# Optimization experiments

Measured on AMD Instinct MI355X. Metric: run time of the kernel, lower is better.

Reference implementation:

```python
import jax, jax.numpy as jnp
import numpy as np

N_NODES = 100000
N_EDGES = 1600000
IN_DIM = 64
HID = 64
N_LAYERS = 2
BN_EPS = 1e-5


def setup_inputs() -> dict:
    key = jax.random.key(0)
    ks = jax.random.split(key, 10)
    s = 0.02
    return {
        "x": jax.random.normal(ks[0], (N_NODES, IN_DIM), dtype=jnp.float32),
        "edge_index": jax.random.randint(ks[1], (2, N_EDGES), 0, N_NODES),
        "edge_attr": jax.random.uniform(ks[2], (N_EDGES,), dtype=jnp.float32),
        "lin_W": jax.random.normal(ks[3], (IN_DIM, HID), dtype=jnp.float32) * s,
        "lin_b": jnp.zeros((HID,), dtype=jnp.float32),
        "eenc_w": jax.random.normal(ks[4], (HID,), dtype=jnp.float32) * s,
        "eenc_b": jnp.zeros((HID,), dtype=jnp.float32),
        "conv_W": jax.random.normal(ks[5], (N_LAYERS, HID, HID), dtype=jnp.float32) * s,
        "conv_b": jnp.zeros((N_LAYERS, HID), dtype=jnp.float32),
        "bn_gamma": jnp.ones((N_LAYERS, HID), dtype=jnp.float32),
        "bn_beta": jnp.zeros((N_LAYERS, HID), dtype=jnp.float32),
    }


def _forward(x, edge_index, edge_attr, lin_W, lin_b, eenc_w, eenc_b,
             conv_W, conv_b, bn_gamma, bn_beta):
    n = x.shape[0]
    src, dst = edge_index[0], edge_index[1]
    # input projection (in_dim > 1 -> lin_layer branch)
    h = x @ lin_W + lin_b                                  # [N, HID]
    e = edge_attr[:, None] * eenc_w[None, :] + eenc_b      # [E, HID]
    h0 = h
    h = h.at[src].set(jax.nn.relu(h0[src] + e))
    h = h.at[dst].set(jax.nn.relu(h0[dst] + e))
    # GCN normalization with self-loops (weight 1), shared across layers
    loops = jnp.arange(n)
    s2 = jnp.concatenate([src, loops])
    d2 = jnp.concatenate([dst, loops])
    w2 = jnp.concatenate([edge_attr, jnp.ones((n,), dtype=h.dtype)])
    deg = jax.ops.segment_sum(w2, d2, num_segments=n)
    dinv = jnp.where(deg > 0, 1.0 / jnp.sqrt(jnp.where(deg > 0, deg, 1.0)), 0.0)
    norm = dinv[s2] * w2 * dinv[d2]                        # [E+N]
    h_list = []
    for l in range(N_LAYERS):
        xw = h @ conv_W[l]                                 # [N, HID]
        agg = jax.ops.segment_sum(norm[:, None] * xw[s2], d2, num_segments=n)
        agg = agg + conv_b[l]
        mean = jnp.mean(agg, axis=0)
        var = jnp.mean((agg - mean) ** 2, axis=0)          # biased, as BN uses
        hn = (agg - mean) / jnp.sqrt(var + BN_EPS) * bn_gamma[l] + bn_beta[l]
        # dropout is identity (eval mode); relu on all but last layer
        h = hn if l == N_LAYERS - 1 else jax.nn.relu(hn)
        h_list.append(h)
    return jnp.concatenate(h_list, axis=1)                 # [N, N_LAYERS*HID]


def reference(x, edge_index, edge_attr, lin_W, lin_b, eenc_w, eenc_b,
              conv_W, conv_b, bn_gamma, bn_beta):
    return _forward(x, edge_index, edge_attr, lin_W, lin_b, eenc_w, eenc_b,
                    conv_W, conv_b, bn_gamma, bn_beta)
```

## Files before the change

### kernel.cpp

```cpp
#include <hip/hip_runtime.h>
#include <hip/hip_fp16.h>

#define N_NODES 100000
#define N_EDGES 1600000
#define BN_EPS 1e-5f
#define NBLK_E 6250
#define NBLK_G 3125
#define NBLK_N 391
#define NBINS 391
#define BCAP 4608
#define PT 4096
#define NPART 391
#define OVF_CAP 32768
#define A18 262144.0f
#define A18_INV 3.814697265625e-6f
typedef unsigned long long ull;
typedef unsigned int uint;


__global__ void init_kernel(int* gcnt, int* win, uint* zbitmap, int* flags, float* bnacc) {
    int v = blockIdx.x * blockDim.x + threadIdx.x;
    if (v < N_NODES) win[v] = -1;
    if (v < NBINS) gcnt[v] = 0;
    if (v < 3125) zbitmap[v] = 0;
    if (v < 2) flags[v] = 0;
    if (v < 256) bnacc[v] = 0.0f;
}

__launch_bounds__(256)
__global__ void partition_gemm(const int* __restrict__ src, const int* __restrict__ dst,
                               const float* __restrict__ attr,
                               ull* __restrict__ bucket, int* __restrict__ gcnt,
                               int* __restrict__ flags, int* __restrict__ ovf_b,
                               ull* __restrict__ ovf_e,
                               const float* __restrict__ x, const float* __restrict__ lin_W,
                               const float* __restrict__ lin_b, float* __restrict__ h0) {
    __shared__ ull ent[PT];
    __shared__ unsigned short ebin[PT];
    __shared__ int hist[NBINS];
    __shared__ int cur[NBINS];
    __shared__ int gdel[NBINS];
    __shared__ int sc[512];
    int t = threadIdx.x;
    if (blockIdx.x < NPART) {
        int e0 = blockIdx.x * PT;
        int n = N_EDGES - e0; if (n > PT) n = PT;
        for (int b = t; b < NBINS; b += 256) hist[b] = 0;
        __syncthreads();
        for (int k = t; k < n; k += 256) atomicAdd(&hist[dst[e0 + k] >> 8], 1);
        __syncthreads();
        sc[t] = (t < NBINS) ? hist[t] : 0;
        sc[t + 256] = (t + 256 < NBINS) ? hist[t + 256] : 0;
        __syncthreads();
        for (int off = 1; off < 512; off <<= 1) {
            int a0 = sc[t] + ((t >= off) ? sc[t - off] : 0);
            int a1 = sc[t + 256] + sc[t + 256 - off];
            __syncthreads();
            sc[t] = a0; sc[t + 256] = a1;
            __syncthreads();
        }
        for (int b = t; b < NBINS; b += 256) {
            int lb = sc[b] - hist[b];
            cur[b] = lb;
            int gb = atomicAdd(&gcnt[b], hist[b]);
            gdel[b] = gb - lb;
        }
        __syncthreads();
        for (int k = t; k < n; k += 256) {
            int i = e0 + k;
            int d = dst[i];
            uint aq = (uint)(attr[i] * A18); if (aq > 0x3FFFFu) aq = 0x3FFFFu;
            int bin = d >> 8;
            ull e = ((ull)(d & 255) << 56) | ((ull)i << 35) | ((ull)src[i] << 18) | aq;
            int p = atomicAdd(&cur[bin], 1);
            ent[p] = e;
            ebin[p] = (unsigned short)bin;
        }
        __syncthreads();
        for (int k = t; k < n; k += 256) {
            int b = ebin[k];
            int off = k + gdel[b];
            if (off < BCAP) bucket[(size_t)b * BCAP + off] = ent[k];
            else {
                int q = atomicAdd(&flags[1], 1);
                if (q < OVF_CAP) { ovf_b[q] = b; ovf_e[q] = ent[k]; }
            }
        }
        return;
    }
    float* xs = (float*)ent;
    int lane = t & 63, w = t >> 6;
    int base = (blockIdx.x - NPART) * 32;
    const float4* Xv = (const float4*)(x + (size_t)base * 64);
    float4* xsv = (float4*)xs;
    xsv[t] = Xv[t];
    xsv[t + 256] = Xv[t + 256];
    float wc[64];
    #pragma unroll
    for (int k = 0; k < 64; ++k) wc[k] = lin_W[k * 64 + lane];
    __syncthreads();
    float bval = lin_b[lane];
    for (int rr = 0; rr < 8; ++rr) {
        int rl = w * 8 + rr;
        const float4* xr = (const float4*)(xs + rl * 64);
        float acc = bval;
        #pragma unroll
        for (int k4 = 0; k4 < 16; ++k4) {
            float4 xv = xr[k4];
            acc = fmaf(xv.x, wc[4 * k4 + 0], acc);
            acc = fmaf(xv.y, wc[4 * k4 + 1], acc);
            acc = fmaf(xv.z, wc[4 * k4 + 2], acc);
            acc = fmaf(xv.w, wc[4 * k4 + 3], acc);
        }
        h0[(size_t)(base + rl) * 64 + lane] = acc;
    }
}

__launch_bounds__(256)
__global__ void finalize_reorder(const ull* __restrict__ bucket, const int* __restrict__ gcnt,
                                 const int* __restrict__ ovf_b, const ull* __restrict__ ovf_e,
                                 int* __restrict__ flags, uint* __restrict__ zbitmap,
                                 float* __restrict__ dinv, float* __restrict__ wa,
                                 ull* __restrict__ csr2, int* __restrict__ startv,
                                 int* __restrict__ lenv) {
    __shared__ ull ent[BCAP];
    __shared__ int cnt[256];
    __shared__ int sc[256];
    __shared__ int cur[256];
    __shared__ int cbase[257];
    int t = threadIdx.x, b = blockIdx.x;
    int len = gcnt[b], blen = len < BCAP ? len : BCAP;
    const ull* bb = bucket + (size_t)b * BCAP;
    cnt[t] = 0;
    __syncthreads();
    ull r[18];
    #pragma unroll
    for (int k = 0; k < 18; ++k) {
        int j = k * 256 + t;
        r[k] = 0;
        if (j < blen) {
            ull e = bb[j];
            r[k] = e;
            atomicAdd(&cnt[(int)(e >> 56)], 1);
        }
    }
    __syncthreads();
    sc[t] = cnt[t];
    __syncthreads();
    for (int off = 1; off < 256; off <<= 1) {
        int a = sc[t] + ((t >= off) ? sc[t - off] : 0);
        __syncthreads();
        sc[t] = a;
        __syncthreads();
    }
    cbase[t + 1] = sc[t];
    if (t == 0) cbase[0] = 0;
    cur[t] = sc[t] - cnt[t];
    __syncthreads();
    #pragma unroll
    for (int k = 0; k < 18; ++k) {
        int j = k * 256 + t;
        if (j < blen) {
            ull e = r[k];
            int p = atomicAdd(&cur[(int)(e >> 56)], 1);
            ent[p] = e;
        }
    }
    __syncthreads();
    size_t base = (size_t)b * BCAP;
    for (int k = t; k < blen; k += 256) {
        ull e = ent[k];
        csr2[base + k] = (((ull)(e & 0x3FFFFull)) << 32) | ((e >> 18) & 0x1FFFFull);
    }
    int j0 = cbase[t], j1 = cbase[t + 1];
    float sum = 0.0f; uint winx = 0, wat = 0;
    for (int j = j0; j < j1; ++j) {
        ull e = ent[j];
        uint aq = (uint)(e & 0x3FFFFull);
        sum += (float)aq * A18_INV;
        uint ei = (uint)((e >> 35) & 0x1FFFFFull) + 1u;
        if (ei > winx) { winx = ei; wat = aq; }
    }
    if (len > BCAP) {
        int oc = flags[1]; if (oc > OVF_CAP) oc = OVF_CAP;
        for (int q = 0; q < oc; ++q) {
            if (ovf_b[q] != b) continue;
            ull e = ovf_e[q];
            if ((int)(e >> 56) != t) continue;
            uint aq = (uint)(e & 0x3FFFFull);
            sum += (float)aq * A18_INV;
            uint ei = (uint)((e >> 35) & 0x1FFFFFull) + 1u;
            if (ei > winx) { winx = ei; wat = aq; }
        }
    }
    int v = b * 256 + t;
    if (v < N_NODES) {
        dinv[v] = rsqrtf(1.0f + sum);
        startv[v] = (int)(base + j0);
        lenv[v] = j1 - j0;
        if (winx > 0) {
            wa[v] = (float)wat * A18_INV;
        } else {
            wa[v] = -1.0f;
            atomicOr(&zbitmap[v >> 5], 1u << (v & 31));
            flags[0] = 1;
        }
    }
}

__global__ void fixup_scan(const int* __restrict__ src, const int* __restrict__ flags,
                           const uint* __restrict__ zbitmap, int* __restrict__ win) {
    if (flags[0] == 0) return;
    int i = blockIdx.x * 256 + threadIdx.x;
    int s = src[i];
    if ((zbitmap[s >> 5] >> (s & 31)) & 1u) atomicMax(&win[s], i);
}

__global__ void fixup_apply(const int* __restrict__ flags, const uint* __restrict__ zbitmap,
                            const int* __restrict__ win, const float* __restrict__ attr,
                            float* __restrict__ wa) {
    if (flags[0] == 0) return;
    int v = blockIdx.x * 256 + threadIdx.x;
    if (v >= N_NODES) return;
    if (((zbitmap[v >> 5] >> (v & 31)) & 1u) && win[v] >= 0) wa[v] = attr[win[v]];
}

__launch_bounds__(256)
__global__ void gemm_l0_nrm(const float* __restrict__ h0, const float* __restrict__ W,
                            const float* __restrict__ wa, const float* __restrict__ ew,
                            const float* __restrict__ eb, __half* __restrict__ xw16,
                            ull* __restrict__ csr2, const int* __restrict__ gcnt,
                            const float* __restrict__ dinv) {
    __shared__ float xs[2048];
    int t = threadIdx.x;
    if (blockIdx.x < NBINS) {
        int b = blockIdx.x;
        int len = gcnt[b], blen = len < BCAP ? len : BCAP;
        ull* c = csr2 + (size_t)b * BCAP;
        for (int k = t; k < blen; k += 256) {
            ull pk = c[k];
            uint s = (uint)pk;
            float np = (float)(uint)(pk >> 32) * A18_INV * dinv[s];
            c[k] = ((ull)__float_as_uint(np) << 32) | s;
        }
        return;
    }
    int lane = t & 63, w = t >> 6;
    int base = (blockIdx.x - NBINS) * 32;
    const float4* Hv = (const float4*)(h0 + (size_t)base * 64);
    #pragma unroll
    for (int q = 0; q < 2; ++q) {
        int idx = t + q * 256;
        int rl = idx >> 4, f0 = (idx & 15) * 4;
        float4 v = Hv[idx];
        float wav = wa[base + rl];
        if (wav >= 0.0f) {
            v.x = fmaxf(fmaf(wav, ew[f0 + 0], v.x + eb[f0 + 0]), 0.0f);
            v.y = fmaxf(fmaf(wav, ew[f0 + 1], v.y + eb[f0 + 1]), 0.0f);
            v.z = fmaxf(fmaf(wav, ew[f0 + 2], v.z + eb[f0 + 2]), 0.0f);
            v.w = fmaxf(fmaf(wav, ew[f0 + 3], v.w + eb[f0 + 3]), 0.0f);
        }
        ((float4*)xs)[idx] = v;
    }
    float wc[64];
    #pragma unroll
    for (int k = 0; k < 64; ++k) wc[k] = W[k * 64 + lane];
    __syncthreads();
    for (int rr = 0; rr < 8; ++rr) {
        int rl = w * 8 + rr;
        const float4* xr = (const float4*)(xs + rl * 64);
        float acc = 0.0f;
        #pragma unroll
        for (int k4 = 0; k4 < 16; ++k4) {
            float4 xv = xr[k4];
            acc = fmaf(xv.x, wc[4 * k4 + 0], acc);
            acc = fmaf(xv.y, wc[4 * k4 + 1], acc);
            acc = fmaf(xv.z, wc[4 * k4 + 2], acc);
            acc = fmaf(xv.w, wc[4 * k4 + 3], acc);
        }
        xw16[(size_t)(base + rl) * 64 + lane] = __float2half(acc);
    }
}

__launch_bounds__(256)
__global__ void gemm_l1(const float* __restrict__ agg, const float* __restrict__ bnacc,
                        const float* __restrict__ gamma, const float* __restrict__ beta,
                        const float* __restrict__ W, float* __restrict__ out,
                        __half* __restrict__ xw16) {
    __shared__ float xs[2048];
    int t = threadIdx.x, lane = t & 63, w = t >> 6;
    int base = blockIdx.x * 32;
    const float4* Av = (const float4*)(agg + (size_t)base * 64);
    const float invN = 1.0f / (float)N_NODES;
    #pragma unroll
    for (int q = 0; q < 2; ++q) {
        int idx = t + q * 256;
        int rl = idx >> 4, f0 = (idx & 15) * 4;
        float4 v = Av[idx];
        float vv[4] = {v.x, v.y, v.z, v.w};
        #pragma unroll
        for (int c = 0; c < 4; ++c) {
            int f = f0 + c;
            float mean = bnacc[f] * invN;
            float var = bnacc[64 + f] * invN - mean * mean;
            float scl = gamma[f] * rsqrtf(var + BN_EPS);
            float bs = beta[f] - mean * scl;
            vv[c] = fmaxf(fmaf(vv[c], scl, bs), 0.0f);
        }
        float4 r = {vv[0], vv[1], vv[2], vv[3]};
        ((float4*)xs)[idx] = r;
        *(float4*)(out + (size_t)(base + rl) * 128 + f0) = r;
    }
    float wc[64];
    #pragma unroll
    for (int k = 0; k < 64; ++k) wc[k] = W[k * 64 + lane];
    __syncthreads();
    for (int rr = 0; rr < 8; ++rr) {
        int rl = w * 8 + rr;
        const float4* xr = (const float4*)(xs + rl * 64);
        float acc = 0.0f;
        #pragma unroll
        for (int k4 = 0; k4 < 16; ++k4) {
            float4 xv = xr[k4];
            acc = fmaf(xv.x, wc[4 * k4 + 0], acc);
            acc = fmaf(xv.y, wc[4 * k4 + 1], acc);
            acc = fmaf(xv.z, wc[4 * k4 + 2], acc);
            acc = fmaf(xv.w, wc[4 * k4 + 3], acc);
        }
        xw16[(size_t)(base + rl) * 64 + lane] = __float2half(acc);
    }
}

__launch_bounds__(256)
__global__ void gather4(const __half* __restrict__ xw16, const ull* __restrict__ csr2,
                        const int* __restrict__ startv, const int* __restrict__ lenv,
                        const float* __restrict__ dinv, const int* __restrict__ gcnt,
                        const int* __restrict__ flags, const int* __restrict__ ovf_b,
                        const ull* __restrict__ ovf_e,
                        const float* __restrict__ convb, float* __restrict__ agg,
                        float* __restrict__ bnacc) {
    __shared__ float reds[4][64];
    __shared__ float redq[4][64];
    int t = threadIdx.x, lane = t & 63, w = t >> 6;
    int ng = lane >> 4, fl = lane & 15, f0 = fl * 4, ngb = ng << 4;
    float cb0 = convb[f0], cb1 = convb[f0 + 1], cb2 = convb[f0 + 2], cb3 = convb[f0 + 3];
    float s0 = 0.f, s1 = 0.f, s2 = 0.f, s3 = 0.f;
    float q0 = 0.f, q1 = 0.f, q2 = 0.f, q3 = 0.f;
    int ovfn = flags[1];
    for (int v = blockIdx.x * 16 + w * 4 + ng; v < N_NODES; v += 32768) {
        float dv = dinv[v];
        int sb = startv[v], ln = lenv[v];
        float2 raw = *(const float2*)(xw16 + (size_t)v * 64 + f0);
        float2 xv01 = __half22float2(*(__half2*)&raw.x);
        float2 xv23 = __half22float2(*(__half2*)&raw.y);
        float w2 = dv * dv;
        float a0 = w2 * xv01.x, a1 = w2 * xv01.y, a2 = w2 * xv23.x, a3 = w2 * xv23.y;
        float b0 = 0.f, b1 = 0.f, b2 = 0.f, b3 = 0.f;
        for (int c0 = 0; c0 < ln; c0 += 16) {
            int m = ln - c0; if (m > 16) m = 16;
            ull pk = (fl < m) ? csr2[sb + c0 + fl] : 0ull;
            int j = 0;
            for (; j + 4 <= m; j += 4) {
                ull pA = __shfl(pk, ngb + j, 64);
                ull pB = __shfl(pk, ngb + j + 1, 64);
                ull pC = __shfl(pk, ngb + j + 2, 64);
                ull pD = __shfl(pk, ngb + j + 3, 64);
                float2 rA = *(const float2*)(xw16 + (size_t)(uint)pA * 64 + f0);
                float2 rB = *(const float2*)(xw16 + (size_t)(uint)pB * 64 + f0);
                float2 rC = *(const float2*)(xw16 + (size_t)(uint)pC * 64 + f0);
                float2 rD = *(const float2*)(xw16 + (size_t)(uint)pD * 64 + f0);
                float nA = __uint_as_float((uint)(pA >> 32)) * dv;
                float nB = __uint_as_float((uint)(pB >> 32)) * dv;
                float nC = __uint_as_float((uint)(pC >> 32)) * dv;
                float nD = __uint_as_float((uint)(pD >> 32)) * dv;
                float2 xA01 = __half22float2(*(__half2*)&rA.x);
                float2 xA23 = __half22float2(*(__half2*)&rA.y);
                float2 xB01 = __half22float2(*(__half2*)&rB.x);
                float2 xB23 = __half22float2(*(__half2*)&rB.y);
                float2 xC01 = __half22float2(*(__half2*)&rC.x);
                float2 xC23 = __half22float2(*(__half2*)&rC.y);
                float2 xD01 = __half22float2(*(__half2*)&rD.x);
                float2 xD23 = __half22float2(*(__half2*)&rD.y);
                a0 = fmaf(nA, xA01.x, a0); a1 = fmaf(nA, xA01.y, a1);
                a2 = fmaf(nA, xA23.x, a2); a3 = fmaf(nA, xA23.y, a3);
                b0 = fmaf(nB, xB01.x, b0); b1 = fmaf(nB, xB01.y, b1);
                b2 = fmaf(nB, xB23.x, b2); b3 = fmaf(nB, xB23.y, b3);
                a0 = fmaf(nC, xC01.x, a0); a1 = fmaf(nC, xC01.y, a1);
                a2 = fmaf(nC, xC23.x, a2); a3 = fmaf(nC, xC23.y, a3);
                b0 = fmaf(nD, xD01.x, b0); b1 = fmaf(nD, xD01.y, b1);
                b2 = fmaf(nD, xD23.x, b2); b3 = fmaf(nD, xD23.y, b3);
            }
            for (; j < m; ++j) {
                ull pA = __shfl(pk, ngb + j, 64);
                float2 rA = *(const float2*)(xw16 + (size_t)(uint)pA * 64 + f0);
                float nA = __uint_as_float((uint)(pA >> 32)) * dv;
                float2 xA01 = __half22float2(*(__half2*)&rA.x);
                float2 xA23 = __half22float2(*(__half2*)&rA.y);
                a0 = fmaf(nA, xA01.x, a0); a1 = fmaf(nA, xA01.y, a1);
                a2 = fmaf(nA, xA23.x, a2); a3 = fmaf(nA, xA23.y, a3);
            }
        }
        float t0 = a0 + b0, t1 = a1 + b1, t2 = a2 + b2, t3 = a3 + b3;
        if (ovfn > 0 && gcnt[v >> 8] > BCAP) {
            int oc = ovfn; if (oc > OVF_CAP) oc = OVF_CAP;
            int ld = v & 255, b = v >> 8;
            for (int q = 0; q < oc; ++q) {
                if (ovf_b[q] != b) continue;
                ull e = ovf_e[q];
                if ((int)(e >> 56) != ld) continue;
                uint s = (uint)((e >> 18) & 0x1FFFFull);
                float nr = (float)(uint)(e & 0x3FFFFull) * A18_INV * dinv[s] * dv;
                float2 rr = *(const float2*)(xw16 + (size_t)s * 64 + f0);
                float2 x01 = __half22float2(*(__half2*)&rr.x);
                float2 x23 = __half22float2(*(__half2*)&rr.y);
                t0 = fmaf(nr, x01.x, t0); t1 = fmaf(nr, x01.y, t1);
                t2 = fmaf(nr, x23.x, t2); t3 = fmaf(nr, x23.y, t3);
            }
        }
        t0 += cb0; t1 += cb1; t2 += cb2; t3 += cb3;
        *(float4*)(agg + (size_t)v * 64 + f0) = make_float4(t0, t1, t2, t3);
        s0 += t0; q0 += t0 * t0;
        s1 += t1; q1 += t1 * t1;
        s2 += t2; q2 += t2 * t2;
        s3 += t3; q3 += t3 * t3;
    }
    s0 += __shfl_xor(s0, 16, 64); s0 += __shfl_xor(s0, 32, 64);
    s1 += __shfl_xor(s1, 16, 64); s1 += __shfl_xor(s1, 32, 64);
    s2 += __shfl_xor(s2, 16, 64); s2 += __shfl_xor(s2, 32, 64);
    s3 += __shfl_xor(s3, 16, 64); s3 += __shfl_xor(s3, 32, 64);
    q0 += __shfl_xor(q0, 16, 64); q0 += __shfl_xor(q0, 32, 64);
    q1 += __shfl_xor(q1, 16, 64); q1 += __shfl_xor(q1, 32, 64);
    q2 += __shfl_xor(q2, 16, 64); q2 += __shfl_xor(q2, 32, 64);
    q3 += __shfl_xor(q3, 16, 64); q3 += __shfl_xor(q3, 32, 64);
    if (ng == 0) {
        reds[w][f0] = s0; reds[w][f0 + 1] = s1; reds[w][f0 + 2] = s2; reds[w][f0 + 3] = s3;
        redq[w][f0] = q0; redq[w][f0 + 1] = q1; redq[w][f0 + 2] = q2; redq[w][f0 + 3] = q3;
    }
    __syncthreads();
    if (t < 64) {
        float ss = reds[0][t] + reds[1][t] + reds[2][t] + reds[3][t];
        float qq = redq[0][t] + redq[1][t] + redq[2][t] + redq[3][t];
        atomicAdd(&bnacc[t], ss);
        atomicAdd(&bnacc[64 + t], qq);
    }
}

__launch_bounds__(256)
__global__ void bn_final(const float* __restrict__ agg, const float* __restrict__ bnacc,
                         const float* __restrict__ gamma, const float* __restrict__ beta,
                         float* __restrict__ out) {
    int idx = blockIdx.x * 256 + threadIdx.x;
    int f0 = (idx & 15) * 4, v = idx >> 4;
    const float invN = 1.0f / (float)N_NODES;
    float4 a = *(const float4*)(agg + (size_t)v * 64 + f0);
    float r[4] = {a.x, a.y, a.z, a.w};
    #pragma unroll
    for (int c = 0; c < 4; ++c) {
        int f = f0 + c;
        float mean = bnacc[f] * invN;
        float var = bnacc[64 + f] * invN - mean * mean;
        float scl = gamma[f] * rsqrtf(var + BN_EPS);
        float bs = beta[f] - mean * scl;
        r[c] = fmaf(r[c], scl, bs);
    }
    *(float4*)(out + (size_t)v * 128 + 64 + f0) = make_float4(r[0], r[1], r[2], r[3]);
}

extern "C" void kernel_launch(void* const* d_in, const int* in_sizes, int n_in,
                              void* d_out, int out_size, void* d_ws, size_t ws_size,
                              hipStream_t stream) {
    const float* x      = (const float*)d_in[0];
    const int*   eidx   = (const int*)d_in[1];
    const float* attr   = (const float*)d_in[2];
    const float* lin_W  = (const float*)d_in[3];
    const float* lin_b  = (const float*)d_in[4];
    const float* eenc_w = (const float*)d_in[5];
    const float* eenc_b = (const float*)d_in[6];
    const float* conv_W = (const float*)d_in[7];
    const float* conv_b = (const float*)d_in[8];
    const float* gamma  = (const float*)d_in[9];
    const float* beta   = (const float*)d_in[10];
    float* out = (float*)d_out;

    const int* src = eidx;
    const int* dst = eidx + N_EDGES;

    char* p = (char*)d_ws;
    ull* bucket = (ull*)p;   p += (size_t)NBINS * BCAP * 8;
    ull* csr2   = (ull*)p;   p += (size_t)NBINS * BCAP * 8;
    ull* ovf_e  = (ull*)p;   p += (size_t)OVF_CAP * 8;
    float* h0   = (float*)p; p += (size_t)N_NODES * 64 * 4;
    __half* xw16 = (__half*)p; p += (size_t)N_NODES * 64 * 2;
    float* dinv = (float*)p; p += (size_t)N_NODES * 4;
    float* wa   = (float*)p; p += (size_t)N_NODES * 4;
    int* win    = (int*)p;   p += (size_t)N_NODES * 4;
    int* startv = (int*)p;   p += (size_t)N_NODES * 4;
    int* lenv   = (int*)p;   p += (size_t)N_NODES * 4;
    int* ovf_b  = (int*)p;   p += (size_t)OVF_CAP * 4;
    int* gcnt   = (int*)p;   p += (NBINS + 1) * 4 + 20;
    uint* zbitmap = (uint*)p; p += 3125 * 4 + 12;
    int* flags  = (int*)p;   p += 64;
    float* bnacc = (float*)p; p += 256 * 4;
    float* agg = h0;

    init_kernel<<<NBLK_N, 256, 0, stream>>>(gcnt, win, zbitmap, flags, bnacc);
    partition_gemm<<<NPART + NBLK_G, 256, 0, stream>>>(src, dst, attr, bucket, gcnt,
                                                       flags, ovf_b, ovf_e,
                                                       x, lin_W, lin_b, h0);
    finalize_reorder<<<NBINS, 256, 0, stream>>>(bucket, gcnt, ovf_b, ovf_e,
                                                flags, zbitmap, dinv, wa,
                                                csr2, startv, lenv);
    fixup_scan<<<NBLK_E, 256, 0, stream>>>(src, flags, zbitmap, win);
    fixup_apply<<<NBLK_N, 256, 0, stream>>>(flags, zbitmap, win, attr, wa);

    gemm_l0_nrm<<<NBINS + NBLK_G, 256, 0, stream>>>(h0, conv_W, wa, eenc_w, eenc_b,
                                                    xw16, csr2, gcnt, dinv);
    gather4<<<2048, 256, 0, stream>>>(xw16, csr2, startv, lenv, dinv, gcnt,
                                      flags, ovf_b, ovf_e, conv_b, agg, bnacc);
    gemm_l1<<<NBLK_G, 256, 0, stream>>>(agg, bnacc, gamma, beta,
                                        conv_W + 64 * 64, out, xw16);
    gather4<<<2048, 256, 0, stream>>>(xw16, csr2, startv, lenv, dinv, gcnt,
                                      flags, ovf_b, ovf_e, conv_b + 64, agg, bnacc + 128);
    bn_final<<<6250, 256, 0, stream>>>(agg, bnacc + 128, gamma + 64, beta + 64, out);
}
```

Baseline: 415.3 us.

## Store h0 and agg intermediates in fp16 and split gather into node-per-thread launches

Intermediate node features h0 and the aggregation buffer are now stored as fp16 instead of fp32, which halves the bytes written and re-read by the GEMM, gather and BN kernels. The gather kernel drops its grid-stride loop: each thread group now handles one node, and the kernel is launched twice over the two halves of the node range. The partition pass keeps the dst indices in registers so they are not loaded twice. The trade-offs are fp16 rounding of pre-BN values, which can cost accuracy, and two extra kernel launches.

Result: slower. 660.9 us (+59.1%).

```diff
diff --git a/kernel.cpp b/kernel.cpp
--- a/kernel.cpp
+++ b/kernel.cpp
@@ -34,7 +34,7 @@
                                int* __restrict__ flags, int* __restrict__ ovf_b,
                                ull* __restrict__ ovf_e,
                                const float* __restrict__ x, const float* __restrict__ lin_W,
-                               const float* __restrict__ lin_b, float* __restrict__ h0) {
+                               const float* __restrict__ lin_b, __half* __restrict__ h0h) {
     __shared__ ull ent[PT];
     __shared__ unsigned short ebin[PT];
     __shared__ int hist[NBINS];
@@ -47,7 +47,14 @@
         int n = N_EDGES - e0; if (n > PT) n = PT;
         for (int b = t; b < NBINS; b += 256) hist[b] = 0;
         __syncthreads();
-        for (int k = t; k < n; k += 256) atomicAdd(&hist[dst[e0 + k] >> 8], 1);
+        int dreg[16];
+        #pragma unroll
+        for (int i2 = 0; i2 < 16; ++i2) {
+            int k = t + i2 * 256;
+            int d = (k < n) ? dst[e0 + k] : -1;
+            dreg[i2] = d;
+            if (d >= 0) atomicAdd(&hist[d >> 8], 1);
+        }
         __syncthreads();
         sc[t] = (t < NBINS) ? hist[t] : 0;
         sc[t + 256] = (t + 256 < NBINS) ? hist[t + 256] : 0;
@@ -66,9 +73,12 @@
             gdel[b] = gb - lb;
         }
         __syncthreads();
-        for (int k = t; k < n; k += 256) {
+        #pragma unroll
+        for (int i2 = 0; i2 < 16; ++i2) {
+            int k = t + i2 * 256;
+            int d = dreg[i2];
+            if (d < 0) continue;
             int i = e0 + k;
-            int d = dst[i];
             uint aq = (uint)(attr[i] * A18); if (aq > 0x3FFFFu) aq = 0x3FFFFu;
             int bin = d >> 8;
             ull e = ((ull)(d & 255) << 56) | ((ull)i << 35) | ((ull)src[i] << 18) | aq;
@@ -112,7 +122,7 @@
             acc = fmaf(xv.z, wc[4 * k4 + 2], acc);
             acc = fmaf(xv.w, wc[4 * k4 + 3], acc);
         }
-        h0[(size_t)(base + rl) * 64 + lane] = acc;
+        h0h[(size_t)(base + rl) * 64 + lane] = __float2half(acc);
     }
 }
 
@@ -226,7 +236,7 @@
 }
 
 __launch_bounds__(256)
-__global__ void gemm_l0_nrm(const float* __restrict__ h0, const float* __restrict__ W,
+__global__ void gemm_l0_nrm(const __half* __restrict__ h0h, const float* __restrict__ W,
                             const float* __restrict__ wa, const float* __restrict__ ew,
                             const float* __restrict__ eb, __half* __restrict__ xw16,
                             ull* __restrict__ csr2, const int* __restrict__ gcnt,
@@ -247,12 +257,15 @@
     }
     int lane = t & 63, w = t >> 6;
     int base = (blockIdx.x - NBINS) * 32;
-    const float4* Hv = (const float4*)(h0 + (size_t)base * 64);
+    const uint2* Hv = (const uint2*)(h0h + (size_t)base * 64);
     #pragma unroll
     for (int q = 0; q < 2; ++q) {
         int idx = t + q * 256;
         int rl = idx >> 4, f0 = (idx & 15) * 4;
-        float4 v = Hv[idx];
+        uint2 hv = Hv[idx];
+        float2 p01 = __half22float2(*(__half2*)&hv.x);
+        float2 p23 = __half22float2(*(__half2*)&hv.y);
+        float4 v = {p01.x, p01.y, p23.x, p23.y};
         float wav = wa[base + rl];
         if (wav >= 0.0f) {
             v.x = fmaxf(fmaf(wav, ew[f0 + 0], v.x + eb[f0 + 0]), 0.0f);
@@ -283,21 +296,23 @@
 }
 
 __launch_bounds__(256)
-__global__ void gemm_l1(const float* __restrict__ agg, const float* __restrict__ bnacc,
+__global__ void gemm_l1(const __half* __restrict__ aggh, const float* __restrict__ bnacc,
                         const float* __restrict__ gamma, const float* __restrict__ beta,
                         const float* __restrict__ W, float* __restrict__ out,
                         __half* __restrict__ xw16) {
     __shared__ float xs[2048];
     int t = threadIdx.x, lane = t & 63, w = t >> 6;
     int base = blockIdx.x * 32;
-    const float4* Av = (const float4*)(agg + (size_t)base * 64);
+    const uint2* Av = (const uint2*)(aggh + (size_t)base * 64);
     const float invN = 1.0f / (float)N_NODES;
     #pragma unroll
     for (int q = 0; q < 2; ++q) {
         int idx = t + q * 256;
         int rl = idx >> 4, f0 = (idx & 15) * 4;
-        float4 v = Av[idx];
-        float vv[4] = {v.x, v.y, v.z, v.w};
+        uint2 hv = Av[idx];
+        float2 p01 = __half22float2(*(__half2*)&hv.x);
+        float2 p23 = __half22float2(*(__half2*)&hv.y);
+        float vv[4] = {p01.x, p01.y, p23.x, p23.y};
         #pragma unroll
         for (int c = 0; c < 4; ++c) {
             int f = f0 + c;
@@ -332,98 +347,97 @@
 }
 
 __launch_bounds__(256)
-__global__ void gather4(const __half* __restrict__ xw16, const ull* __restrict__ csr2,
+__global__ void gather4(int vbase,
+                        const __half* __restrict__ xw16, const ull* __restrict__ csr2,
                         const int* __restrict__ startv, const int* __restrict__ lenv,
                         const float* __restrict__ dinv, const int* __restrict__ gcnt,
                         const int* __restrict__ flags, const int* __restrict__ ovf_b,
                         const ull* __restrict__ ovf_e,
-                        const float* __restrict__ convb, float* __restrict__ agg,
+                        const float* __restrict__ convb, __half* __restrict__ aggh,
                         float* __restrict__ bnacc) {
     __shared__ float reds[4][64];
     __shared__ float redq[4][64];
     int t = threadIdx.x, lane = t & 63, w = t >> 6;
     int ng = lane >> 4, fl = lane & 15, f0 = fl * 4, ngb = ng << 4;
-    float cb0 = convb[f0], cb1 = convb[f0 + 1], cb2 = convb[f0 + 2], cb3 = convb[f0 + 3];
-    float s0 = 0.f, s1 = 0.f, s2 = 0.f, s3 = 0.f;
-    float q0 = 0.f, q1 = 0.f, q2 = 0.f, q3 = 0.f;
+    int v = vbase + blockIdx.x * 16 + w * 4 + ng;
+    float dv = dinv[v];
+    int sb = startv[v], ln = lenv[v];
+    float2 raw = *(const float2*)(xw16 + (size_t)v * 64 + f0);
+    float2 xv01 = __half22float2(*(__half2*)&raw.x);
+    float2 xv23 = __half22float2(*(__half2*)&raw.y);
+    float w2 = dv * dv;
+    float a0 = w2 * xv01.x, a1 = w2 * xv01.y, a2 = w2 * xv23.x, a3 = w2 * xv23.y;
+    float b0 = 0.f, b1 = 0.f, b2 = 0.f, b3 = 0.f;
+    for (int c0 = 0; c0 < ln; c0 += 16) {
+        int m = ln - c0; if (m > 16) m = 16;
+        ull pk = (fl < m) ? csr2[sb + c0 + fl] : 0ull;
+        int j = 0;
+        for (; j + 4 <= m; j += 4) {
+            ull pA = __shfl(pk, ngb + j, 64);
+            ull pB = __shfl(pk, ngb + j + 1, 64);
+            ull pC = __shfl(pk, ngb + j + 2, 64);
+            ull pD = __shfl(pk, ngb + j + 3, 64);
+            float2 rA = *(const float2*)(xw16 + (size_t)(uint)pA * 64 + f0);
+            float2 rB = *(const float2*)(xw16 + (size_t)(uint)pB * 64 + f0);
+            float2 rC = *(const float2*)(xw16 + (size_t)(uint)pC * 64 + f0);
+            float2 rD = *(const float2*)(xw16 + (size_t)(uint)pD * 64 + f0);
+            float nA = __uint_as_float((uint)(pA >> 32)) * dv;
+            float nB = __uint_as_float((uint)(pB >> 32)) * dv;
+            float nC = __uint_as_float((uint)(pC >> 32)) * dv;
+            float nD = __uint_as_float((uint)(pD >> 32)) * dv;
+            float2 xA01 = __half22float2(*(__half2*)&rA.x);
+            float2 xA23 = __half22float2(*(__half2*)&rA.y);
+            float2 xB01 = __half22float2(*(__half2*)&rB.x);
+            float2 xB23 = __half22float2(*(__half2*)&rB.y);
+            float2 xC01 = __half22float2(*(__half2*)&rC.x);
+            float2 xC23 = __half22float2(*(__half2*)&rC.y);
+            float2 xD01 = __half22float2(*(__half2*)&rD.x);
+            float2 xD23 = __half22float2(*(__half2*)&rD.y);
+            a0 = fmaf(nA, xA01.x, a0); a1 = fmaf(nA, xA01.y, a1);
+            a2 = fmaf(nA, xA23.x, a2); a3 = fmaf(nA, xA23.y, a3);
+            b0 = fmaf(nB, xB01.x, b0); b1 = fmaf(nB, xB01.y, b1);
+            b2 = fmaf(nB, xB23.x, b2); b3 = fmaf(nB, xB23.y, b3);
+            a0 = fmaf(nC, xC01.x, a0); a1 = fmaf(nC, xC01.y, a1);
+            a2 = fmaf(nC, xC23.x, a2); a3 = fmaf(nC, xC23.y, a3);
+            b0 = fmaf(nD, xD01.x, b0); b1 = fmaf(nD, xD01.y, b1);
+            b2 = fmaf(nD, xD23.x, b2); b3 = fmaf(nD, xD23.y, b3);
+        }
+        for (; j < m; ++j) {
+            ull pA = __shfl(pk, ngb + j, 64);
+            float2 rA = *(const float2*)(xw16 + (size_t)(uint)pA * 64 + f0);
+            float nA = __uint_as_float((uint)(pA >> 32)) * dv;
+            float2 xA01 = __half22float2(*(__half2*)&rA.x);
+            float2 xA23 = __half22float2(*(__half2*)&rA.y);
+            a0 = fmaf(nA, xA01.x, a0); a1 = fmaf(nA, xA01.y, a1);
+            a2 = fmaf(nA, xA23.x, a2); a3 = fmaf(nA, xA23.y, a3);
+        }
+    }
+    float t0 = a0 + b0, t1 = a1 + b1, t2 = a2 + b2, t3 = a3 + b3;
     int ovfn = flags[1];
-    for (int v = blockIdx.x * 16 + w * 4 + ng; v < N_NODES; v += 32768) {
-        float dv = dinv[v];
-        int sb = startv[v], ln = lenv[v];
-        float2 raw = *(const float2*)(xw16 + (size_t)v * 64 + f0);
-        float2 xv01 = __half22float2(*(__half2*)&raw.x);
-        float2 xv23 = __half22float2(*(__half2*)&raw.y);
-        float w2 = dv * dv;
-        float a0 = w2 * xv01.x, a1 = w2 * xv01.y, a2 = w2 * xv23.x, a3 = w2 * xv23.y;
-        float b0 = 0.f, b1 = 0.f, b2 = 0.f, b3 = 0.f;
-        for (int c0 = 0; c0 < ln; c0 += 16) {
-            int m = ln - c0; if (m > 16) m = 16;
-            ull pk = (fl < m) ? csr2[sb + c0 + fl] : 0ull;
-            int j = 0;
-            for (; j + 4 <= m; j += 4) {
-                ull pA = __shfl(pk, ngb + j, 64);
-                ull pB = __shfl(pk, ngb + j + 1, 64);
-                ull pC = __shfl(pk, ngb + j + 2, 64);
-                ull pD = __shfl(pk, ngb + j + 3, 64);
-                float2 rA = *(const float2*)(xw16 + (size_t)(uint)pA * 64 + f0);
-                float2 rB = *(const float2*)(xw16 + (size_t)(uint)pB * 64 + f0);
-                float2 rC = *(const float2*)(xw16 + (size_t)(uint)pC * 64 + f0);
-                float2 rD = *(const float2*)(xw16 + (size_t)(uint)pD * 64 + f0);
-                float nA = __uint_as_float((uint)(pA >> 32)) * dv;
-                float nB = __uint_as_float((uint)(pB >> 32)) * dv;
-                float nC = __uint_as_float((uint)(pC >> 32)) * dv;
-                float nD = __uint_as_float((uint)(pD >> 32)) * dv;
-                float2 xA01 = __half22float2(*(__half2*)&rA.x);
-                float2 xA23 = __half22float2(*(__half2*)&rA.y);
-                float2 xB01 = __half22float2(*(__half2*)&rB.x);
-                float2 xB23 = __half22float2(*(__half2*)&rB.y);
-                float2 xC01 = __half22float2(*(__half2*)&rC.x);
-                float2 xC23 = __half22float2(*(__half2*)&rC.y);
-                float2 xD01 = __half22float2(*(__half2*)&rD.x);
-                float2 xD23 = __half22float2(*(__half2*)&rD.y);
-                a0 = fmaf(nA, xA01.x, a0); a1 = fmaf(nA, xA01.y, a1);
-                a2 = fmaf(nA, xA23.x, a2); a3 = fmaf(nA, xA23.y, a3);
-                b0 = fmaf(nB, xB01.x, b0); b1 = fmaf(nB, xB01.y, b1);
-                b2 = fmaf(nB, xB23.x, b2); b3 = fmaf(nB, xB23.y, b3);
-                a0 = fmaf(nC, xC01.x, a0); a1 = fmaf(nC, xC01.y, a1);
-                a2 = fmaf(nC, xC23.x, a2); a3 = fmaf(nC, xC23.y, a3);
-                b0 = fmaf(nD, xD01.x, b0); b1 = fmaf(nD, xD01.y, b1);
-                b2 = fmaf(nD, xD23.x, b2); b3 = fmaf(nD, xD23.y, b3);
-            }
-            for (; j < m; ++j) {
-                ull pA = __shfl(pk, ngb + j, 64);
-                float2 rA = *(const float2*)(xw16 + (size_t)(uint)pA * 64 + f0);
-                float nA = __uint_as_float((uint)(pA >> 32)) * dv;
-                float2 xA01 = __half22float2(*(__half2*)&rA.x);
-                float2 xA23 = __half22float2(*(__half2*)&rA.y);
-                a0 = fmaf(nA, xA01.x, a0); a1 = fmaf(nA, xA01.y, a1);
-                a2 = fmaf(nA, xA23.x, a2); a3 = fmaf(nA, xA23.y, a3);
-            }
-        }
-        float t0 = a0 + b0, t1 = a1 + b1, t2 = a2 + b2, t3 = a3 + b3;
-        if (ovfn > 0 && gcnt[v >> 8] > BCAP) {
-            int oc = ovfn; if (oc > OVF_CAP) oc = OVF_CAP;
-            int ld = v & 255, b = v >> 8;
-            for (int q = 0; q < oc; ++q) {
-                if (ovf_b[q] != b) continue;
-                ull e = ovf_e[q];
-                if ((int)(e >> 56) != ld) continue;
-                uint s = (uint)((e >> 18) & 0x1FFFFull);
-                float nr = (float)(uint)(e & 0x3FFFFull) * A18_INV * dinv[s] * dv;
-                float2 rr = *(const float2*)(xw16 + (size_t)s * 64 + f0);
-                float2 x01 = __half22float2(*(__half2*)&rr.x);
-                float2 x23 = __half22float2(*(__half2*)&rr.y);
-                t0 = fmaf(nr, x01.x, t0); t1 = fmaf(nr, x01.y, t1);
-                t2 = fmaf(nr, x23.x, t2); t3 = fmaf(nr, x23.y, t3);
-            }
-        }
-        t0 += cb0; t1 += cb1; t2 += cb2; t3 += cb3;
-        *(float4*)(agg + (size_t)v * 64 + f0) = make_float4(t0, t1, t2, t3);
-        s0 += t0; q0 += t0 * t0;
-        s1 += t1; q1 += t1 * t1;
-        s2 += t2; q2 += t2 * t2;
-        s3 += t3; q3 += t3 * t3;
-    }
+    if (ovfn > 0 && gcnt[v >> 8] > BCAP) {
+        int oc = ovfn; if (oc > OVF_CAP) oc = OVF_CAP;
+        int ld = v & 255, b = v >> 8;
+        for (int q = 0; q < oc; ++q) {
+            if (ovf_b[q] != b) continue;
+            ull e = ovf_e[q];
+            if ((int)(e >> 56) != ld) continue;
+            uint s = (uint)((e >> 18) & 0x1FFFFull);
+            float nr = (float)(uint)(e & 0x3FFFFull) * A18_INV * dinv[s] * dv;
+            float2 rr = *(const float2*)(xw16 + (size_t)s * 64 + f0);
+            float2 x01 = __half22float2(*(__half2*)&rr.x);
+            float2 x23 = __half22float2(*(__half2*)&rr.y);
+            t0 = fmaf(nr, x01.x, t0); t1 = fmaf(nr, x01.y, t1);
+            t2 = fmaf(nr, x23.x, t2); t3 = fmaf(nr, x23.y, t3);
+        }
+    }
+    float4 cb = *(const float4*)(convb + f0);
+    t0 += cb.x; t1 += cb.y; t2 += cb.z; t3 += cb.w;
+    __half2 h01 = __floats2half2_rn(t0, t1);
+    __half2 h23 = __floats2half2_rn(t2, t3);
+    uint2 st; st.x = *(uint*)&h01; st.y = *(uint*)&h23;
+    *(uint2*)(aggh + (size_t)v * 64 + f0) = st;
+    float s0 = t0, s1 = t1, s2 = t2, s3 = t3;
+    float q0 = t0 * t0, q1 = t1 * t1, q2 = t2 * t2, q3 = t3 * t3;
     s0 += __shfl_xor(s0, 16, 64); s0 += __shfl_xor(s0, 32, 64);
     s1 += __shfl_xor(s1, 16, 64); s1 += __shfl_xor(s1, 32, 64);
     s2 += __shfl_xor(s2, 16, 64); s2 += __shfl_xor(s2, 32, 64);
@@ -446,14 +460,16 @@
 }
 
 __launch_bounds__(256)
-__global__ void bn_final(const float* __restrict__ agg, const float* __restrict__ bnacc,
+__global__ void bn_final(const __half* __restrict__ aggh, const float* __restrict__ bnacc,
                          const float* __restrict__ gamma, const float* __restrict__ beta,
                          float* __restrict__ out) {
     int idx = blockIdx.x * 256 + threadIdx.x;
     int f0 = (idx & 15) * 4, v = idx >> 4;
     const float invN = 1.0f / (float)N_NODES;
-    float4 a = *(const float4*)(agg + (size_t)v * 64 + f0);
-    float r[4] = {a.x, a.y, a.z, a.w};
+    uint2 hv = *(const uint2*)(aggh + (size_t)v * 64 + f0);
+    float2 p01 = __half22float2(*(__half2*)&hv.x);
+    float2 p23 = __half22float2(*(__half2*)&hv.y);
+    float r[4] = {p01.x, p01.y, p23.x, p23.y};
     #pragma unroll
     for (int c = 0; c < 4; ++c) {
         int f = f0 + c;
@@ -489,7 +505,7 @@
     ull* bucket = (ull*)p;   p += (size_t)NBINS * BCAP * 8;
     ull* csr2   = (ull*)p;   p += (size_t)NBINS * BCAP * 8;
     ull* ovf_e  = (ull*)p;   p += (size_t)OVF_CAP * 8;
-    float* h0   = (float*)p; p += (size_t)N_NODES * 64 * 4;
+    __half* h0h = (__half*)p; p += (size_t)N_NODES * 64 * 4;
     __half* xw16 = (__half*)p; p += (size_t)N_NODES * 64 * 2;
     float* dinv = (float*)p; p += (size_t)N_NODES * 4;
     float* wa   = (float*)p; p += (size_t)N_NODES * 4;
@@ -501,25 +517,29 @@
     uint* zbitmap = (uint*)p; p += 3125 * 4 + 12;
     int* flags  = (int*)p;   p += 64;
     float* bnacc = (float*)p; p += 256 * 4;
-    float* agg = h0;
+    __half* aggh = h0h;
 
     init_kernel<<<NBLK_N, 256, 0, stream>>>(gcnt, win, zbitmap, flags, bnacc);
     partition_gemm<<<NPART + NBLK_G, 256, 0, stream>>>(src, dst, attr, bucket, gcnt,
                                                        flags, ovf_b, ovf_e,
-                                                       x, lin_W, lin_b, h0);
+                                                       x, lin_W, lin_b, h0h);
     finalize_reorder<<<NBINS, 256, 0, stream>>>(bucket, gcnt, ovf_b, ovf_e,
                                                 flags, zbitmap, dinv, wa,
                                                 csr2, startv, lenv);
     fixup_scan<<<NBLK_E, 256, 0, stream>>>(src, flags, zbitmap, win);
     fixup_apply<<<NBLK_N, 256, 0, stream>>>(flags, zbitmap, win, attr, wa);
 
-    gemm_l0_nrm<<<NBINS + NBLK_G, 256, 0, stream>>>(h0, conv_W, wa, eenc_w, eenc_b,
+    gemm_l0_nrm<<<NBINS + NBLK_G, 256, 0, stream>>>(h0h, conv_W, wa, eenc_w, eenc_b,
                                                     xw16, csr2, gcnt, dinv);
-    gather4<<<2048, 256, 0, stream>>>(xw16, csr2, startv, lenv, dinv, gcnt,
-                                      flags, ovf_b, ovf_e, conv_b, agg, bnacc);
-    gemm_l1<<<NBLK_G, 256, 0, stream>>>(agg, bnacc, gamma, beta,
+    gather4<<<3125, 256, 0, stream>>>(0, xw16, csr2, startv, lenv, dinv, gcnt,
+                                      flags, ovf_b, ovf_e, conv_b, aggh, bnacc);
+    gather4<<<3125, 256, 0, stream>>>(50000, xw16, csr2, startv, lenv, dinv, gcnt,
+                                      flags, ovf_b, ovf_e, conv_b, aggh, bnacc);
+    gemm_l1<<<NBLK_G, 256, 0, stream>>>(aggh, bnacc, gamma, beta,
                                         conv_W + 64 * 64, out, xw16);
-    gather4<<<2048, 256, 0, stream>>>(xw16, csr2, startv, lenv, dinv, gcnt,
-                                      flags, ovf_b, ovf_e, conv_b + 64, agg, bnacc + 128);
-    bn_final<<<6250, 256, 0, stream>>>(agg, bnacc + 128, gamma + 64, beta + 64, out);
-}
+    gather4<<<3125, 256, 0, stream>>>(0, xw16, csr2, startv, lenv, dinv, gcnt,
+                                      flags, ovf_b, ovf_e, conv_b + 64, aggh, bnacc + 128);
+    gather4<<<3125, 256, 0, stream>>>(50000, xw16, csr2, startv, lenv, dinv, gcnt,
+                                      flags, ovf_b, ovf_e, conv_b + 64, aggh, bnacc + 128);
+    bn_final<<<6250, 256, 0, stream>>>(aggh, bnacc + 128, gamma + 64, beta + 64, out);
+}
```
